# Kernel tuning notes

Hardware: AMD Instinct MI355X
Metric: run time of the kernel (lower is better)

## Reference

```python
import jax, jax.numpy as jnp
import numpy as np

W0 = 30.0  # SIREN frequency


def setup_inputs() -> dict:
    key = jax.random.key(0)
    ks = jax.random.split(key, 8)
    B, N, IN, OUT, C, H, W = 4, 65536, 2, 512, 64, 32, 32
    # coordinates in [-1, 1]
    x = jax.random.uniform(ks[0], (B, N, IN), minval=-1.0, maxval=1.0, dtype=jnp.float32)
    latent = jax.random.normal(ks[1], (B, C, H, W), dtype=jnp.float32)
    v = jax.random.normal(ks[2], (B, C, H, W), dtype=jnp.float32)
    # SIREN first-layer init: uniform(-1/in, 1/in)
    w_std = 1.0 / IN
    W_lin = jax.random.uniform(ks[3], (OUT, IN), minval=-w_std, maxval=w_std, dtype=jnp.float32)
    b_lin = jax.random.uniform(ks[4], (OUT,), minval=-w_std, maxval=w_std, dtype=jnp.float32)
    # 1x1 conv weights (kernel dims squeezed): [OUT, C]
    W_shift = jax.random.normal(ks[5], (OUT, C), dtype=jnp.float32) * 0.05
    b_shift = jax.random.normal(ks[6], (OUT,), dtype=jnp.float32) * 0.05
    W_vshift = jax.random.normal(ks[7], (OUT, C), dtype=jnp.float32) * 0.05
    b_vshift = jnp.zeros((OUT,), dtype=jnp.float32)
    return dict(x=x, latent=latent, v=v, W_lin=W_lin, b_lin=b_lin,
                W_shift=W_shift, b_shift=b_shift, W_vshift=W_vshift, b_vshift=b_vshift)


def _gather_nearest(feat_hwc, coords):
    # feat_hwc: [B, H, W, C]; coords: [B, N, >=2] with values ~[-1, 1]
    B, H, W, _ = feat_hwc.shape
    ix = jnp.clip(jnp.round((coords[..., 0] + 1.0) / 2.0 * (W - 1)).astype(jnp.int32), 0, W - 1)
    iy = jnp.clip(jnp.round((coords[..., 1] + 1.0) / 2.0 * (H - 1)).astype(jnp.int32), 0, H - 1)
    return feat_hwc[jnp.arange(B)[:, None], iy, ix]  # [B, N, C]


def reference(x, latent, v, W_lin, b_lin, W_shift, b_shift, W_vshift, b_vshift):
    # Linear: [B, N, IN] -> [B, N, OUT]
    h = jnp.einsum('bni,oi->bno', x, W_lin) + b_lin
    # 1x1 convs -> channels-last feature maps [B, H, W, OUT]
    shift = jnp.einsum('bchw,oc->bhwo', latent, W_shift) + b_shift
    shift_v = jnp.einsum('bchw,oc->bhwo', v, W_vshift) + b_vshift
    # nearest-neighbor gathers using h's first two channels as coordinates
    patch = _gather_nearest(shift, h)
    patch_v = _gather_nearest(shift_v, h)
    # scale = 1.0 (modulate_scale=False); shift modulation then sin activation
    return jnp.sin(W0 * (h + patch + patch_v))
```

## Files before the change

kernel.cpp:

```cpp
#include <hip/hip_runtime.h>
#include <math.h>

#define SIREN_W0 30.0f

typedef float f32x4 __attribute__((ext_vector_type(4)));
typedef float f32x2 __attribute__((ext_vector_type(2)));

__global__ __launch_bounds__(256) void build_combined(
    const float* __restrict__ latent, const float* __restrict__ v,
    const float* __restrict__ W_shift, const float* __restrict__ b_shift,
    const float* __restrict__ W_vshift, const float* __restrict__ b_vshift,
    float* __restrict__ combined)
{
    __shared__ float featL[16][64];
    __shared__ float featV[16][64];
    const int pos0 = blockIdx.x * 16;
    const int b    = pos0 >> 10;
    const int rem  = pos0 & 1023;
    const int t    = threadIdx.x;

    const float* latBase = latent + (size_t)b * 65536 + rem;
    const float* vBase   = v      + (size_t)b * 65536 + rem;
#pragma unroll
    for (int k = 0; k < 4; ++k) {
        int e = t + k * 256;
        int c = e >> 4, p = e & 15;
        featL[p][c] = latBase[c * 1024 + p];
        featV[p][c] = vBase[c * 1024 + p];
    }
    __syncthreads();

    const int og = t & 127;
    const int pg = t >> 7;
    const int o0 = og * 4;
    const int p0 = pg * 8;

    float acc[8][4];
#pragma unroll
    for (int j = 0; j < 4; ++j) {
        float binit = b_shift[o0 + j] + b_vshift[o0 + j];
#pragma unroll
        for (int p = 0; p < 8; ++p) acc[p][j] = binit;
    }

    const f32x4* WS = (const f32x4*)(W_shift  + (size_t)o0 * 64);
    const f32x4* WV = (const f32x4*)(W_vshift + (size_t)o0 * 64);

#pragma unroll 4
    for (int c4 = 0; c4 < 16; ++c4) {
        f32x4 wS[4], wV[4];
#pragma unroll
        for (int j = 0; j < 4; ++j) {
            wS[j] = WS[j * 16 + c4];
            wV[j] = WV[j * 16 + c4];
        }
#pragma unroll
        for (int p = 0; p < 8; ++p) {
            f32x4 fL = *(const f32x4*)&featL[p0 + p][c4 * 4];
            f32x4 fV = *(const f32x4*)&featV[p0 + p][c4 * 4];
#pragma unroll
            for (int j = 0; j < 4; ++j) {
                acc[p][j] += fL.x * wS[j].x + fL.y * wS[j].y
                           + fL.z * wS[j].z + fL.w * wS[j].w
                           + fV.x * wV[j].x + fV.y * wV[j].y
                           + fV.z * wV[j].z + fV.w * wV[j].w;
            }
        }
    }

#pragma unroll
    for (int p = 0; p < 8; ++p) {
        f32x4 r = { acc[p][0], acc[p][1], acc[p][2], acc[p][3] };
        *(f32x4*)(combined + (size_t)(pos0 + p0 + p) * 512 + o0) = r;
    }
}

__global__ __launch_bounds__(256) void siren_out(
    const float* __restrict__ x, const float* __restrict__ W_lin,
    const float* __restrict__ b_lin, const float* __restrict__ combined,
    float* __restrict__ out)
{
    const int tid   = blockIdx.x * 256 + threadIdx.x;
    const int point = tid >> 5;
    const int lane  = tid & 31;
    const int b     = point >> 16;

    const f32x2 xv = *(const f32x2*)(x + (size_t)point * 2);

    const f32x4 wl = *(const f32x4*)W_lin;
    const f32x2 bl = *(const f32x2*)b_lin;
    const float h0 = xv.x * wl.x + xv.y * wl.y + bl.x;
    const float h1 = xv.x * wl.z + xv.y * wl.w + bl.y;

    const float fx = (h0 + 1.0f) * 0.5f * 31.0f;
    const float fy = (h1 + 1.0f) * 0.5f * 31.0f;
    int ix = (int)rintf(fx); ix = ix < 0 ? 0 : (ix > 31 ? 31 : ix);
    int iy = (int)rintf(fy); iy = iy < 0 ? 0 : (iy > 31 ? 31 : iy);

    const f32x4* crow =
        (const f32x4*)(combined + (size_t)(((b << 5) + iy) * 32 + ix) * 512);
    const f32x4* Wl4 = (const f32x4*)W_lin;
    const f32x4* Bl4 = (const f32x4*)b_lin;
    f32x4* orow = ((f32x4*)out) + (size_t)point * 128;

#pragma unroll
    for (int k = 0; k < 4; ++k) {
        const int chunk = lane + k * 32;
        const f32x4 c4 = crow[chunk];
        const f32x4 wA = Wl4[chunk * 2];
        const f32x4 wB = Wl4[chunk * 2 + 1];
        const f32x4 bb = Bl4[chunk];

        f32x4 r;
        r.x = __sinf(SIREN_W0 * (xv.x * wA.x + xv.y * wA.y + bb.x + c4.x));
        r.y = __sinf(SIREN_W0 * (xv.x * wA.z + xv.y * wA.w + bb.y + c4.y));
        r.z = __sinf(SIREN_W0 * (xv.x * wB.x + xv.y * wB.y + bb.z + c4.z));
        r.w = __sinf(SIREN_W0 * (xv.x * wB.z + xv.y * wB.w + bb.w + c4.w));

        __builtin_nontemporal_store(r, orow + chunk);
    }
}

extern "C" void kernel_launch(void* const* d_in, const int* in_sizes, int n_in,
                              void* d_out, int out_size, void* d_ws, size_t ws_size,
                              hipStream_t stream) {
    const float* x        = (const float*)d_in[0];
    const float* latent   = (const float*)d_in[1];
    const float* v        = (const float*)d_in[2];
    const float* W_lin    = (const float*)d_in[3];
    const float* b_lin    = (const float*)d_in[4];
    const float* W_shift  = (const float*)d_in[5];
    const float* b_shift  = (const float*)d_in[6];
    const float* W_vshift = (const float*)d_in[7];
    const float* b_vshift = (const float*)d_in[8];
    float* out      = (float*)d_out;
    float* combined = (float*)d_ws;

    build_combined<<<256, 256, 0, stream>>>(latent, v, W_shift, b_shift,
                                            W_vshift, b_vshift, combined);

    siren_out<<<32768, 256, 0, stream>>>(x, W_lin, b_lin, combined, out);
}
```

Before: 115.3 us.

## Bucket points by gather cell so output blocks reuse cached combined rows

Adds a counting-sort pipeline (zero counters, atomic histogram over cells, single-block scan, atomic scatter) that groups points by their nearest-neighbor cell. The output kernel then walks the sorted list with a block swizzle, so consecutive warps read the same 2 KB combined row and hit in cache more often. In exchange it adds four extra launches and atomic traffic. Output writes become scattered per point rather than sequential, which may hurt store efficiency.

New measurement: 312.9 us. 171% more time.

```diff
diff --git a/kernel.cpp b/kernel.cpp
--- a/kernel.cpp
+++ b/kernel.cpp
@@ -5,6 +5,26 @@
 
 typedef float f32x4 __attribute__((ext_vector_type(4)));
 typedef float f32x2 __attribute__((ext_vector_type(2)));
+typedef unsigned int u32;
+typedef u32 u32x4 __attribute__((ext_vector_type(4)));
+
+__device__ __forceinline__ int cell_of(const float* __restrict__ x,
+                                       const float* __restrict__ W_lin,
+                                       const float* __restrict__ b_lin,
+                                       int point)
+{
+    const f32x2 xv = *(const f32x2*)(x + (size_t)point * 2);
+    const f32x4 wl = *(const f32x4*)W_lin;
+    const f32x2 bl = *(const f32x2*)b_lin;
+    const float h0 = xv.x * wl.x + xv.y * wl.y + bl.x;
+    const float h1 = xv.x * wl.z + xv.y * wl.w + bl.y;
+    const float fx = (h0 + 1.0f) * 0.5f * 31.0f;
+    const float fy = (h1 + 1.0f) * 0.5f * 31.0f;
+    int ix = (int)rintf(fx); ix = ix < 0 ? 0 : (ix > 31 ? 31 : ix);
+    int iy = (int)rintf(fy); iy = iy < 0 ? 0 : (iy > 31 ? 31 : iy);
+    const int b = point >> 16;
+    return ((b << 5) + iy) * 32 + ix;
+}
 
 __global__ __launch_bounds__(256) void build_combined(
     const float* __restrict__ latent, const float* __restrict__ v,
@@ -75,33 +95,73 @@
     }
 }
 
-__global__ __launch_bounds__(256) void siren_out(
+__global__ __launch_bounds__(256) void zero_counters(u32* __restrict__ buf)
+{
+    int i = blockIdx.x * 256 + threadIdx.x;
+    buf[i] = 0;
+}
+
+__global__ __launch_bounds__(256) void count_cells(
+    const float* __restrict__ x, const float* __restrict__ W_lin,
+    const float* __restrict__ b_lin, u32* __restrict__ counts)
+{
+    const int p = blockIdx.x * 256 + threadIdx.x;
+    atomicAdd(&counts[cell_of(x, W_lin, b_lin, p)], 1u);
+}
+
+__global__ __launch_bounds__(1024) void scan_cells(
+    const u32* __restrict__ counts, u32* __restrict__ cursors)
+{
+    const int t = threadIdx.x;
+    u32x4 c = ((const u32x4*)counts)[t];
+    u32 tot = c.x + c.y + c.z + c.w;
+    __shared__ u32 sc[1024];
+    sc[t] = tot;
+    __syncthreads();
+#pragma unroll
+    for (int off = 1; off < 1024; off <<= 1) {
+        u32 v = (t >= off) ? sc[t - off] : 0u;
+        __syncthreads();
+        sc[t] += v;
+        __syncthreads();
+    }
+    u32 base = sc[t] - tot;
+    u32x4 s;
+    s.x = base; s.y = s.x + c.x; s.z = s.y + c.y; s.w = s.z + c.z;
+    ((u32x4*)cursors)[t] = s;
+}
+
+__global__ __launch_bounds__(256) void scatter_points(
+    const float* __restrict__ x, const float* __restrict__ W_lin,
+    const float* __restrict__ b_lin, u32* __restrict__ cursors,
+    u32* __restrict__ sorted)
+{
+    const int p = blockIdx.x * 256 + threadIdx.x;
+    const int cell = cell_of(x, W_lin, b_lin, p);
+    const u32 slot = atomicAdd(&cursors[cell], 1u);
+    sorted[slot] = (u32)p | ((u32)cell << 18);
+}
+
+__global__ __launch_bounds__(256) void siren_out_sorted(
     const float* __restrict__ x, const float* __restrict__ W_lin,
     const float* __restrict__ b_lin, const float* __restrict__ combined,
-    float* __restrict__ out)
-{
-    const int tid   = blockIdx.x * 256 + threadIdx.x;
-    const int point = tid >> 5;
-    const int lane  = tid & 31;
-    const int b     = point >> 16;
-
-    const f32x2 xv = *(const f32x2*)(x + (size_t)point * 2);
-
-    const f32x4 wl = *(const f32x4*)W_lin;
-    const f32x2 bl = *(const f32x2*)b_lin;
-    const float h0 = xv.x * wl.x + xv.y * wl.y + bl.x;
-    const float h1 = xv.x * wl.z + xv.y * wl.w + bl.y;
-
-    const float fx = (h0 + 1.0f) * 0.5f * 31.0f;
-    const float fy = (h1 + 1.0f) * 0.5f * 31.0f;
-    int ix = (int)rintf(fx); ix = ix < 0 ? 0 : (ix > 31 ? 31 : ix);
-    int iy = (int)rintf(fy); iy = iy < 0 ? 0 : (iy > 31 ? 31 : iy);
-
-    const f32x4* crow =
-        (const f32x4*)(combined + (size_t)(((b << 5) + iy) * 32 + ix) * 512);
-    const f32x4* Wl4 = (const f32x4*)W_lin;
-    const f32x4* Bl4 = (const f32x4*)b_lin;
-    f32x4* orow = ((f32x4*)out) + (size_t)point * 128;
+    const u32* __restrict__ sorted, float* __restrict__ out)
+{
+    const int bid = blockIdx.x;
+    const int pb  = (bid & 7) * 4096 + (bid >> 3);
+
+    const int t    = threadIdx.x;
+    const int lane = t & 31;
+    const u32 entry = sorted[pb * 8 + (t >> 5)];
+    const int p    = (int)(entry & 262143u);
+    const int cell = (int)(entry >> 18);
+
+    const f32x2 xv = *(const f32x2*)(x + (size_t)p * 2);
+
+    const f32x4* crow = (const f32x4*)(combined + (size_t)cell * 512);
+    const f32x4* Wl4  = (const f32x4*)W_lin;
+    const f32x4* Bl4  = (const f32x4*)b_lin;
+    f32x4* orow = ((f32x4*)out) + (size_t)p * 128;
 
 #pragma unroll
     for (int k = 0; k < 4; ++k) {
@@ -133,11 +193,20 @@
     const float* b_shift  = (const float*)d_in[6];
     const float* W_vshift = (const float*)d_in[7];
     const float* b_vshift = (const float*)d_in[8];
-    float* out      = (float*)d_out;
-    float* combined = (float*)d_ws;
-
-    build_combined<<<256, 256, 0, stream>>>(latent, v, W_shift, b_shift,
-                                            W_vshift, b_vshift, combined);
-
-    siren_out<<<32768, 256, 0, stream>>>(x, W_lin, b_lin, combined, out);
-}
+    float* out = (float*)d_out;
+
+    char* ws = (char*)d_ws;
+    float* combined = (float*)ws;
+    u32*   counts   = (u32*)(ws + (8u << 20));
+    u32*   cursors  = (u32*)(ws + (8u << 20) + (16u << 10));
+    u32*   sorted   = (u32*)(ws + (8u << 20) + (64u << 10));
+
+    zero_counters <<<32,    256, 0, stream>>>(counts);
+    build_combined<<<256,   256, 0, stream>>>(latent, v, W_shift, b_shift,
+                                              W_vshift, b_vshift, combined);
+    count_cells   <<<1024,  256, 0, stream>>>(x, W_lin, b_lin, counts);
+    scan_cells    <<<1,    1024, 0, stream>>>(counts, cursors);
+    scatter_points<<<1024,  256, 0, stream>>>(x, W_lin, b_lin, cursors, sorted);
+    siren_out_sorted<<<32768, 256, 0, stream>>>(x, W_lin, b_lin, combined,
+                                                sorted, out);
+}
```
